# Kernel optimization log

Hardware: AMD Instinct MI355X
Metric: run time of the kernel (lower is better)

## Reference

```python
import jax, jax.numpy as jnp
from jax import lax
import numpy as np

IMG_H = IMG_W = 1024
STRIDE = 16
FH = FW = 64
C = 512
NA = 9
IOU_T = 0.7
NEG = -1e30
NUM_CLASSES = 21
FV = 4096
POOL = 7


def _make_anchor_map():
    scales = np.array([128.0, 256.0, 512.0])
    ratios = np.array([0.5, 1.0, 2.0])
    ah = (scales[:, None] * np.sqrt(ratios)[None, :]).reshape(-1)  # (9,)
    aw = (scales[:, None] / np.sqrt(ratios)[None, :]).reshape(-1)
    cy = (np.arange(FH) + 0.5) * STRIDE
    cx = (np.arange(FW) + 0.5) * STRIDE
    amap = np.zeros((FH, FW, NA, 4), np.float32)
    amap[..., 0] = cy[:, None, None]
    amap[..., 1] = cx[None, :, None]
    amap[..., 2] = ah
    amap[..., 3] = aw
    return amap.reshape(FH, FW, NA * 4)


def setup_inputs() -> dict:
    key = jax.random.key(0)
    ks = jax.random.split(key, 10)
    flat = POOL * POOL * C
    return {
        "feature_map": jax.random.normal(ks[0], (1, C, FH, FW), jnp.float32),
        "anchor_map": jnp.asarray(_make_anchor_map()),
        "anchor_valid_map": jnp.ones((FH, FW, NA), jnp.float32),
        "rpn_conv1_w": 0.01 * jax.random.normal(ks[1], (C, C, 3, 3), jnp.float32),
        "rpn_conv1_b": jnp.zeros((C,), jnp.float32),
        "rpn_cls_w": 0.01 * jax.random.normal(ks[2], (NA, C, 1, 1), jnp.float32),
        "rpn_cls_b": jnp.zeros((NA,), jnp.float32),
        "rpn_box_w": 0.01 * jax.random.normal(ks[3], (NA * 4, C, 1, 1), jnp.float32),
        "rpn_box_b": jnp.zeros((NA * 4,), jnp.float32),
        "fc1_w": 0.01 * jax.random.normal(ks[4], (FV, flat), jnp.float32),
        "fc1_b": jnp.zeros((FV,), jnp.float32),
        "fc2_w": 0.01 * jax.random.normal(ks[5], (FV, FV), jnp.float32),
        "fc2_b": jnp.zeros((FV,), jnp.float32),
        "cls_w": 0.01 * jax.random.normal(ks[6], (NUM_CLASSES, FV), jnp.float32),
        "cls_b": jnp.zeros((NUM_CLASSES,), jnp.float32),
        "reg_w": 0.001 * jax.random.normal(ks[7], (4 * (NUM_CLASSES - 1), FV), jnp.float32),
        "reg_b": jnp.zeros((4 * (NUM_CLASSES - 1),), jnp.float32),
        "max_proposals_pre_nms": 6000,
        "max_proposals_post_nms": 300,
    }


def _conv(x, w, b):
    y = lax.conv_general_dilated(x, w, (1, 1), 'SAME',
                                 dimension_numbers=('NCHW', 'OIHW', 'NCHW'))
    return y + b[None, :, None, None]


def _roi_pool(fm, rois):
    # fm: (C,H,W); rois: (N,4) as (x1,y1,x2,y2) in pixel coords (torchvision RoIPool semantics)
    Hh, Ww = fm.shape[1], fm.shape[2]
    s = 1.0 / STRIDE
    p = jnp.arange(POOL, dtype=fm.dtype)
    hi = jnp.arange(Hh, dtype=fm.dtype)
    wi = jnp.arange(Ww, dtype=fm.dtype)

    def one(roi):
        x1 = jnp.round(roi[0] * s); y1 = jnp.round(roi[1] * s)
        x2 = jnp.round(roi[2] * s); y2 = jnp.round(roi[3] * s)
        rw = jnp.maximum(x2 - x1 + 1.0, 1.0)
        rh = jnp.maximum(y2 - y1 + 1.0, 1.0)
        bh = rh / POOL; bw = rw / POOL
        hstart = jnp.clip(jnp.floor(p * bh) + y1, 0, Hh)
        hend = jnp.clip(jnp.ceil((p + 1) * bh) + y1, 0, Hh)
        wstart = jnp.clip(jnp.floor(p * bw) + x1, 0, Ww)
        wend = jnp.clip(jnp.ceil((p + 1) * bw) + x1, 0, Ww)
        mh = (hi[None, :] >= hstart[:, None]) & (hi[None, :] < hend[:, None])  # (7,H)
        mw = (wi[None, :] >= wstart[:, None]) & (wi[None, :] < wend[:, None])  # (7,W)
        # max over w per (c,h,pw), then max over h per (c,ph,pw)
        t1 = jnp.max(jnp.where(mw[None, None, :, :], fm[:, :, None, :], NEG), axis=-1)  # (C,H,7)
        t2 = jnp.max(jnp.where(mh[None, :, :, None], t1[:, None, :, :], NEG), axis=2)   # (C,7,7)
        return jnp.where(t2 < NEG / 2, 0.0, t2)  # empty bins -> 0

    return lax.map(one, rois)  # (N,C,7,7)


def reference(feature_map, anchor_map, anchor_valid_map,
              rpn_conv1_w, rpn_conv1_b, rpn_cls_w, rpn_cls_b, rpn_box_w, rpn_box_b,
              fc1_w, fc1_b, fc2_w, fc2_b, cls_w, cls_b, reg_w, reg_b,
              max_proposals_pre_nms, max_proposals_post_nms):
    # ---- RPN heads ----
    y = jax.nn.relu(_conv(feature_map, rpn_conv1_w, rpn_conv1_b))
    scores_map = jax.nn.sigmoid(_conv(y, rpn_cls_w, rpn_cls_b)).transpose(0, 2, 3, 1)   # (1,H,W,9)
    deltas_map = _conv(y, rpn_box_w, rpn_box_b).transpose(0, 2, 3, 1)                   # (1,H,W,36)

    # ---- proposals from anchors + deltas (allow_edge_proposals=True: keep all) ----
    anchors = anchor_map.reshape(-1, 4)        # (cy,cx,h,w)
    scores = scores_map.reshape(-1)
    deltas = deltas_map.reshape(-1, 4)         # (ty,tx,th,tw)
    ctr = anchors[:, 0:2] + deltas[:, 0:2] * anchors[:, 2:4]
    sz = anchors[:, 2:4] * jnp.exp(deltas[:, 2:4])
    boxes = jnp.concatenate([ctr - 0.5 * sz, ctr + 0.5 * sz], axis=1)  # (y1,x1,y2,x2)
    hi_clip = jnp.array([IMG_H - 1, IMG_W - 1, IMG_H - 1, IMG_W - 1], boxes.dtype)
    boxes = jnp.clip(boxes, 0.0, hi_clip)

    # ---- top-k pre-NMS ----
    sc_pre, idx = lax.top_k(scores, max_proposals_pre_nms)
    bx = boxes[idx]

    # ---- NMS (IoU 0.7), score-sorted sequential suppression ----
    area = (bx[:, 2] - bx[:, 0]) * (bx[:, 3] - bx[:, 1])
    yy1 = jnp.maximum(bx[:, None, 0], bx[None, :, 0])
    xx1 = jnp.maximum(bx[:, None, 1], bx[None, :, 1])
    yy2 = jnp.minimum(bx[:, None, 2], bx[None, :, 2])
    xx2 = jnp.minimum(bx[:, None, 3], bx[None, :, 3])
    inter = jnp.clip(yy2 - yy1, 0.0) * jnp.clip(xx2 - xx1, 0.0)
    iou = inter / (area[:, None] + area[None, :] - inter + 1e-8)
    n = max_proposals_pre_nms
    jidx = jnp.arange(n)

    def body(i, sup):
        return sup | ((~sup[i]) & (iou[i] > IOU_T) & (jidx > i))

    sup = lax.fori_loop(0, n, body, jnp.zeros((n,), bool))
    kept_scores = jnp.where(sup, -jnp.inf, sc_pre)
    _, idx2 = lax.top_k(kept_scores, max_proposals_post_nms)
    proposals = lax.stop_gradient(bx[idx2])  # (N,4) (y1,x1,y2,x2); detached as in original

    # ---- detector head: RoIPool + FC stack ----
    rois = proposals[:, jnp.array([1, 0, 3, 2])]       # -> (x1,y1,x2,y2)
    pooled = _roi_pool(feature_map[0], rois)           # (N,C,7,7)
    flat = pooled.reshape(pooled.shape[0], -1)
    h1 = jax.nn.relu(flat @ fc1_w.T + fc1_b)
    h2 = jax.nn.relu(h1 @ fc2_w.T + fc2_b)
    classes = jax.nn.softmax(h2 @ cls_w.T + cls_b, axis=1)          # (N,21)
    box_deltas = h2 @ reg_w.T + reg_b                               # (N,80)
    return (scores_map, deltas_map, proposals, classes, box_deltas)
```

## Files before the change

kernel.cpp:

```cpp
#include <hip/hip_runtime.h>
#include <stdint.h>

typedef float f32x4 __attribute__((ext_vector_type(4)));
typedef short s16x8 __attribute__((ext_vector_type(8)));
typedef unsigned long long u64;

__device__ __forceinline__ unsigned short f2bf(float f) {
  union { float f; unsigned u; } v; v.f = f;
  unsigned u = v.u;
  return (unsigned short)((u + 0x7FFFu + ((u >> 16) & 1u)) >> 16);
}
__device__ __forceinline__ float bf2f(unsigned short b) {
  union { unsigned u; float f; } v; v.u = ((unsigned)b) << 16; return v.f;
}

#define CONV_ICC 8
__global__ __launch_bounds__(256, 2) void k_conv3(const float* __restrict__ fm,
                                                  const float* __restrict__ w,
                                                  float* __restrict__ ypart) {
  __shared__ float Xs[CONV_ICC * 342];
  __shared__ float Ws[CONV_ICC * 9 * 64];
  int bid = blockIdx.x;
  int s = bid & 3, ocg = (bid >> 2) & 7, sp = bid >> 5;
  int h0 = (sp >> 2) * 16, w0 = (sp & 3) * 16;
  int oc0 = ocg * 64;
  int t = threadIdx.x;
  int g = t >> 5, p = t & 31;
  int row = p >> 1, colb = (p & 1) * 8;
  float acc[8][8] = {};
  int cbase = s * 128;
  for (int chunk = 0; chunk < 16; chunk++) {
    int c0 = cbase + chunk * CONV_ICC;
    for (int idx = t; idx < CONV_ICC * 324; idx += 256) {
      int ic = idx / 324, rem = idx - ic * 324;
      int r = rem / 18, cc = rem - r * 18;
      int gy = h0 + r - 1, gx = w0 + cc - 1;
      float v = 0.f;
      if ((unsigned)gy < 64u && (unsigned)gx < 64u) v = fm[(c0 + ic) * 4096 + gy * 64 + gx];
      Xs[ic * 342 + r * 19 + cc] = v;
    }
    for (int idx = t; idx < CONV_ICC * 9 * 64; idx += 256) {
      int oc = idx & 63, rest = idx >> 6;
      int ic = rest / 9, k = rest - ic * 9;
      Ws[idx] = w[(u64)(oc0 + oc) * 4608 + (c0 + ic) * 9 + k];
    }
    __syncthreads();
    for (int ic = 0; ic < CONV_ICC; ic++) {
      const float* xb = &Xs[ic * 342 + colb];
      float xr[3][10];
      #pragma unroll
      for (int r = 0; r < 3; r++)
        #pragma unroll
        for (int j = 0; j < 10; j++)
          xr[r][j] = xb[(row + r) * 19 + j];
      #pragma unroll
      for (int kh = 0; kh < 3; kh++) {
        #pragma unroll
        for (int kw = 0; kw < 3; kw++) {
          const float* wp = &Ws[(ic * 9 + kh * 3 + kw) * 64 + g * 8];
          f32x4 wa = *(const f32x4*)wp;
          f32x4 wb = *(const f32x4*)(wp + 4);
          float wv[8] = {wa.x, wa.y, wa.z, wa.w, wb.x, wb.y, wb.z, wb.w};
          #pragma unroll
          for (int o = 0; o < 8; o++) {
            #pragma unroll
            for (int j = 0; j < 8; j++) {
              acc[o][j] += wv[o] * xr[kh][kw + j];
            }
          }
        }
      }
    }
    __syncthreads();
  }
  float* yp = ypart + (u64)s * 2097152;
  #pragma unroll
  for (int j = 0; j < 8; j++) {
    int pxg = (h0 + row) * 64 + (w0 + colb + j);
    f32x4 v0, v1;
    v0.x = acc[0][j]; v0.y = acc[1][j]; v0.z = acc[2][j]; v0.w = acc[3][j];
    v1.x = acc[4][j]; v1.y = acc[5][j]; v1.z = acc[6][j]; v1.w = acc[7][j];
    f32x4* dst = (f32x4*)&yp[(u64)pxg * 512 + oc0 + g * 8];
    dst[0] = v0; dst[1] = v1;
  }
}

__global__ __launch_bounds__(256) void k_rpn1x1(const float* __restrict__ ypart,
                                                const float* __restrict__ conv_b,
                                                const float* __restrict__ cw, const float* __restrict__ cb,
                                                const float* __restrict__ bw, const float* __restrict__ bb,
                                                float* __restrict__ out_s, float* __restrict__ out_d) {
  __shared__ float Ys[16 * 516];
  int px0 = blockIdx.x * 16;
  int t = threadIdx.x;
  for (int c = t; c < 16 * 128; c += 256) {
    int p = c >> 7, seg = c & 127;
    u64 off = (u64)(px0 + p) * 512 + seg * 4;
    f32x4 v0 = *(const f32x4*)&ypart[off];
    f32x4 v1 = *(const f32x4*)&ypart[2097152 + off];
    f32x4 v2 = *(const f32x4*)&ypart[2 * 2097152 + off];
    f32x4 v3 = *(const f32x4*)&ypart[3 * (u64)2097152 + off];
    f32x4 b = *(const f32x4*)&conv_b[seg * 4];
    f32x4 r;
    r.x = fmaxf(v0.x + v1.x + v2.x + v3.x + b.x, 0.f);
    r.y = fmaxf(v0.y + v1.y + v2.y + v3.y + b.y, 0.f);
    r.z = fmaxf(v0.z + v1.z + v2.z + v3.z + b.z, 0.f);
    r.w = fmaxf(v0.w + v1.w + v2.w + v3.w + b.w, 0.f);
    *(f32x4*)&Ys[p * 516 + seg * 4] = r;
  }
  __syncthreads();
  int px = t & 15, og = t >> 4;
  const float* yr = &Ys[px * 516];
  for (int n = og; n < 45; n += 16) {
    const float* wr = (n < 9) ? &cw[n * 512] : &bw[(n - 9) * 512];
    float acc = 0.f;
    for (int k = 0; k < 512; k += 4) {
      f32x4 wv = *(const f32x4*)&wr[k];
      acc += wv.x * yr[k] + wv.y * yr[k + 1] + wv.z * yr[k + 2] + wv.w * yr[k + 3];
    }
    int gpx = px0 + px;
    if (n < 9) {
      float s = acc + cb[n];
      out_s[gpx * 9 + n] = 1.f / (1.f + expf(-s));
    } else {
      out_d[gpx * 36 + (n - 9)] = acc + bb[n - 9];
    }
  }
}

__global__ void k_decode(const float* __restrict__ sc, const float* __restrict__ dl,
                         const float* __restrict__ amap,
                         float* __restrict__ boxes, u64* __restrict__ keys) {
  int i = blockIdx.x * 256 + threadIdx.x;
  if (i >= 65536) return;
  if (i < 36864) {
    int px = i / 9, a = i - px * 9;
    const float* A = &amap[i * 4];
    const float* D = &dl[px * 36 + a * 4];
    float cy = A[0] + D[0] * A[2];
    float cx = A[1] + D[1] * A[3];
    float hh = A[2] * expf(D[2]);
    float ww = A[3] * expf(D[3]);
    float y1 = fminf(fmaxf(cy - 0.5f * hh, 0.f), 1023.f);
    float x1 = fminf(fmaxf(cx - 0.5f * ww, 0.f), 1023.f);
    float y2 = fminf(fmaxf(cy + 0.5f * hh, 0.f), 1023.f);
    float x2 = fminf(fmaxf(cx + 0.5f * ww, 0.f), 1023.f);
    f32x4 v; v.x = y1; v.y = x1; v.z = y2; v.w = x2;
    *(f32x4*)&boxes[i * 4] = v;
    unsigned bits = __float_as_uint(sc[i]);
    u64 key = ((u64)bits << 16) | (u64)(0xFFFFu - (unsigned)i);
    keys[i] = ~key;
  } else {
    keys[i] = ~0ull;
  }
}

__global__ __launch_bounds__(1024) void k_sort_local(u64* __restrict__ keys) {
  __shared__ u64 S[8192];
  int base = blockIdx.x * 8192;
  for (int i = threadIdx.x; i < 8192; i += 1024) S[i] = keys[base + i];
  __syncthreads();
  for (int k = 2; k <= 8192; k <<= 1) {
    for (int j = k >> 1; j > 0; j >>= 1) {
      for (int p = threadIdx.x; p < 4096; p += 1024) {
        int i = ((p & ~(j - 1)) << 1) | (p & (j - 1));
        int ix = i | j;
        bool up = (((base + i) & k) == 0);
        u64 a = S[i], c = S[ix];
        if ((a > c) == up) { S[i] = c; S[ix] = a; }
      }
      __syncthreads();
    }
  }
  for (int i = threadIdx.x; i < 8192; i += 1024) keys[base + i] = S[i];
}

__global__ void k_sort_global(u64* __restrict__ keys, int k, int j) {
  int p = blockIdx.x * 256 + threadIdx.x;
  int i = ((p & ~(j - 1)) << 1) | (p & (j - 1));
  int ix = i | j;
  bool up = ((i & k) == 0);
  u64 a = keys[i], c = keys[ix];
  if ((a > c) == up) { keys[i] = c; keys[ix] = a; }
}

__global__ __launch_bounds__(1024) void k_sort_merge(u64* __restrict__ keys, int k) {
  __shared__ u64 S[8192];
  int base = blockIdx.x * 8192;
  for (int i = threadIdx.x; i < 8192; i += 1024) S[i] = keys[base + i];
  __syncthreads();
  for (int j = 4096; j > 0; j >>= 1) {
    for (int p = threadIdx.x; p < 4096; p += 1024) {
      int i = ((p & ~(j - 1)) << 1) | (p & (j - 1));
      int ix = i | j;
      bool up = (((base + i) & k) == 0);
      u64 a = S[i], c = S[ix];
      if ((a > c) == up) { S[i] = c; S[ix] = a; }
    }
    __syncthreads();
  }
  for (int i = threadIdx.x; i < 8192; i += 1024) keys[base + i] = S[i];
}

__global__ void k_gather_sorted(const u64* __restrict__ keys, const float* __restrict__ boxes,
                                float* __restrict__ bx) {
  int p = blockIdx.x * 256 + threadIdx.x;
  if (p >= 6000) return;
  u64 key = ~keys[p];
  int idx = 0xFFFF - (int)(key & 0xFFFFull);
  *(f32x4*)&bx[p * 4] = *(const f32x4*)&boxes[idx * 4];
}

__global__ __launch_bounds__(128) void k_nms_mask(const float* __restrict__ bx, u64* __restrict__ mask) {
  int i = blockIdx.x;
  int w = threadIdx.x;
  if (w >= 94) return;
  f32x4 bi = *(const f32x4*)&bx[i * 4];
  float ai = (bi.z - bi.x) * (bi.w - bi.y);
  u64 m = 0;
  int j0 = w * 64;
  for (int b = 0; b < 64; b++) {
    int j = j0 + b;
    if (j >= 6000) break;
    if (j <= i) continue;
    f32x4 bj = *(const f32x4*)&bx[j * 4];
    float yy1 = fmaxf(bi.x, bj.x), xx1 = fmaxf(bi.y, bj.y);
    float yy2 = fminf(bi.z, bj.z), xx2 = fminf(bi.w, bj.w);
    float inter = fmaxf(yy2 - yy1, 0.f) * fmaxf(xx2 - xx1, 0.f);
    float aj = (bj.z - bj.x) * (bj.w - bj.y);
    float iou = inter / (ai + aj - inter + 1e-8f);
    if (iou > 0.7f) m |= (1ull << b);
  }
  mask[i * 94 + w] = m;
}

__global__ __launch_bounds__(64) void k_nms_scan(const u64* __restrict__ mask, int* __restrict__ sel) {
  int lane = threadIdx.x;
  u64 rem0 = 0, rem1 = 0;
  int nkeep = 0;
  u64 cur0[16], cur1[16], nxt0[16], nxt1[16];
  bool l30 = (lane < 30);
  #pragma unroll
  for (int r = 0; r < 16; r++) {
    cur0[r] = mask[r * 94 + lane];
    cur1[r] = l30 ? mask[r * 94 + 64 + lane] : 0ull;
  }
  for (int c0 = 0; c0 < 6000; c0 += 16) {
    int n0 = c0 + 16;
    if (n0 < 6000) {
      #pragma unroll
      for (int r = 0; r < 16; r++) {
        nxt0[r] = mask[(n0 + r) * 94 + lane];
        nxt1[r] = l30 ? mask[(n0 + r) * 94 + 64 + lane] : 0ull;
      }
    }
    #pragma unroll
    for (int r = 0; r < 16; r++) {
      int i = c0 + r;
      int wi = i >> 6, bi = i & 63;
      u64 wv = (wi < 64) ? __shfl(rem0, wi, 64) : __shfl(rem1, wi - 64, 64);
      if (!((wv >> bi) & 1ull)) {
        if (lane == 0 && nkeep < 300) sel[nkeep] = i;
        nkeep++;
        rem0 |= cur0[r]; rem1 |= cur1[r];
      }
    }
    if (nkeep >= 300) return;
    #pragma unroll
    for (int r = 0; r < 16; r++) { cur0[r] = nxt0[r]; cur1[r] = nxt1[r]; }
  }
  __shared__ u64 remS[94];
  remS[lane] = rem0;
  if (l30) remS[64 + lane] = rem1;
  __syncthreads();
  if (lane == 0) {
    int k = nkeep;
    for (int i = 0; i < 6000 && k < 300; i++) {
      if ((remS[i >> 6] >> (i & 63)) & 1ull) sel[k++] = i;
    }
  }
}

__global__ void k_gather_prop(const int* __restrict__ sel, const float* __restrict__ bx,
                              float* __restrict__ out_p, float* __restrict__ rois) {
  int r = blockIdx.x * 64 + threadIdx.x;
  if (r >= 300) return;
  int p = sel[r];
  float y1 = bx[p * 4 + 0], x1 = bx[p * 4 + 1], y2 = bx[p * 4 + 2], x2 = bx[p * 4 + 3];
  out_p[r * 4 + 0] = y1; out_p[r * 4 + 1] = x1; out_p[r * 4 + 2] = y2; out_p[r * 4 + 3] = x2;
  rois[r * 4 + 0] = x1; rois[r * 4 + 1] = y1; rois[r * 4 + 2] = x2; rois[r * 4 + 3] = y2;
}

__global__ __launch_bounds__(256) void k_roipool(const float* __restrict__ fm,
                                                 const float* __restrict__ rois,
                                                 unsigned short* __restrict__ pooled) {
  int roi = blockIdx.x / 98;
  int seg = blockIdx.x - roi * 98;
  __shared__ int hs[7], he[7], wls[7], wle[7];
  if (threadIdx.x < 28) {
    int kind = threadIdx.x / 7, p = threadIdx.x - kind * 7;
    float x1 = rintf(rois[roi * 4 + 0] * 0.0625f);
    float y1 = rintf(rois[roi * 4 + 1] * 0.0625f);
    float x2 = rintf(rois[roi * 4 + 2] * 0.0625f);
    float y2 = rintf(rois[roi * 4 + 3] * 0.0625f);
    float rw = fmaxf(x2 - x1 + 1.f, 1.f), rh = fmaxf(y2 - y1 + 1.f, 1.f);
    float bh = rh / 7.f, bw = rw / 7.f;
    float fp = (float)p;
    if (kind == 0) hs[p]  = (int)fminf(fmaxf(floorf(fp * bh) + y1, 0.f), 64.f);
    if (kind == 1) he[p]  = (int)fminf(fmaxf(ceilf((fp + 1.f) * bh) + y1, 0.f), 64.f);
    if (kind == 2) wls[p] = (int)fminf(fmaxf(floorf(fp * bw) + x1, 0.f), 64.f);
    if (kind == 3) wle[p] = (int)fminf(fmaxf(ceilf((fp + 1.f) * bw) + x1, 0.f), 64.f);
  }
  __syncthreads();
  int o = seg * 256 + threadIdx.x;
  int c = o / 49; int cell = o - c * 49;
  int ph = cell / 7, pw = cell - ph * 7;
  int y0 = hs[ph], y1e = he[ph], x0 = wls[pw], x1e = wle[pw];
  bool any = (y1e > y0) && (x1e > x0);
  float m = -1e30f;
  const float* base = &fm[c * 4096];
  for (int yy = y0; yy < y1e; yy++)
    for (int xx = x0; xx < x1e; xx++)
      m = fmaxf(m, base[yy * 64 + xx]);
  pooled[(u64)roi * 25088 + o] = f2bf(any ? m : 0.f);
}

__global__ __launch_bounds__(512) void k_gemm(const unsigned short* __restrict__ A,
                                              const float* __restrict__ B,
                                              float* __restrict__ Cpre,
                                              int K, int Kslice, int N) {
  __shared__ unsigned short As[320 * 40];
  int n0 = blockIdx.x * 128;
  int s = blockIdx.y;
  int t = threadIdx.x;
  int wave = t >> 6, lane = t & 63;
  int mg = wave & 1, ng = wave >> 1;
  int m0 = mg * 160;
  int n0w = n0 + ng * 32;
  int lr = lane & 15, lk = lane >> 4;
  f32x4 acc[10][2];
  #pragma unroll
  for (int mt = 0; mt < 10; mt++)
    for (int nt = 0; nt < 2; nt++) { acc[mt][nt].x = 0; acc[mt][nt].y = 0; acc[mt][nt].z = 0; acc[mt][nt].w = 0; }
  int kbeg = s * Kslice, kend = kbeg + Kslice;
  for (int k0 = kbeg; k0 < kend; k0 += 32) {
    for (int c = t; c < 1280; c += 512) {
      int m = c >> 2, seg = (c & 3) * 8;
      *(uint4*)&As[m * 40 + seg] = *(const uint4*)&A[(u64)m * K + k0 + seg];
    }
    __syncthreads();
    s16x8 bfrag[2];
    #pragma unroll
    for (int nt = 0; nt < 2; nt++) {
      const float* bp = &B[(u64)(n0w + nt * 16 + lr) * K + k0 + lk * 8];
      f32x4 b0 = *(const f32x4*)bp;
      f32x4 b1 = *(const f32x4*)(bp + 4);
      s16x8 f;
      f[0] = (short)f2bf(b0.x); f[1] = (short)f2bf(b0.y); f[2] = (short)f2bf(b0.z); f[3] = (short)f2bf(b0.w);
      f[4] = (short)f2bf(b1.x); f[5] = (short)f2bf(b1.y); f[6] = (short)f2bf(b1.z); f[7] = (short)f2bf(b1.w);
      bfrag[nt] = f;
    }
    #pragma unroll
    for (int mt = 0; mt < 10; mt++) {
      s16x8 afrag = *(const s16x8*)&As[(m0 + mt * 16 + lr) * 40 + lk * 8];
      acc[mt][0] = __builtin_amdgcn_mfma_f32_16x16x32_bf16(afrag, bfrag[0], acc[mt][0], 0, 0, 0);
      acc[mt][1] = __builtin_amdgcn_mfma_f32_16x16x32_bf16(afrag, bfrag[1], acc[mt][1], 0, 0, 0);
    }
    __syncthreads();
  }
  #pragma unroll
  for (int mt = 0; mt < 10; mt++)
    for (int nt = 0; nt < 2; nt++)
      for (int r = 0; r < 4; r++) {
        int m = m0 + mt * 16 + lk * 4 + r;
        int n = n0w + nt * 16 + lr;
        atomicAdd(&Cpre[(u64)m * N + n], acc[mt][nt][r]);
      }
}

__global__ void k_bias_relu_bf(const float* __restrict__ pre, const float* __restrict__ bias,
                               unsigned short* __restrict__ outb) {
  int i = blockIdx.x * 256 + threadIdx.x;
  float v = pre[i] + bias[i & 4095];
  outb[i] = f2bf(fmaxf(v, 0.f));
}

__global__ __launch_bounds__(128) void k_head(const unsigned short* __restrict__ h2,
                                              const float* __restrict__ cw, const float* __restrict__ cb,
                                              const float* __restrict__ rw, const float* __restrict__ rb,
                                              float* __restrict__ out_cls, float* __restrict__ out_reg) {
  __shared__ float Hs[4096];
  __shared__ float logits[101];
  __shared__ float es[21];
  int r = blockIdx.x, t = threadIdx.x;
  for (int c = t; c < 512; c += 128) {
    uint4 raw = *(const uint4*)&h2[(u64)r * 4096 + c * 8];
    unsigned short* sp = (unsigned short*)&raw;
    #pragma unroll
    for (int q = 0; q < 8; q++) Hs[c * 8 + q] = bf2f(sp[q]);
  }
  __syncthreads();
  for (int n = t; n < 101; n += 128) {
    const float* wrow = (n < 21) ? &cw[n * 4096] : &rw[(n - 21) * 4096];
    float acc = 0.f;
    for (int k = 0; k < 4096; k += 4) {
      f32x4 wv = *(const f32x4*)&wrow[k];
      acc += wv.x * Hs[k] + wv.y * Hs[k + 1] + wv.z * Hs[k + 2] + wv.w * Hs[k + 3];
    }
    acc += (n < 21) ? cb[n] : rb[n - 21];
    logits[n] = acc;
  }
  __syncthreads();
  if (t < 21) {
    float mx = logits[0];
    for (int q = 1; q < 21; q++) mx = fmaxf(mx, logits[q]);
    es[t] = expf(logits[t] - mx);
  }
  __syncthreads();
  if (t < 21) {
    float sum = 0.f;
    for (int q = 0; q < 21; q++) sum += es[q];
    out_cls[r * 21 + t] = es[t] / sum;
  }
  if (t >= 21 && t < 101) out_reg[r * 80 + (t - 21)] = logits[t];
}

extern "C" void kernel_launch(void* const* d_in, const int* in_sizes, int n_in,
                              void* d_out, int out_size, void* d_ws, size_t ws_size,
                              hipStream_t stream) {
  (void)in_sizes; (void)n_in; (void)out_size; (void)ws_size;
  const float* fm     = (const float*)d_in[0];
  const float* amap   = (const float*)d_in[1];
  const float* conv_w = (const float*)d_in[3];
  const float* conv_b = (const float*)d_in[4];
  const float* cls_w  = (const float*)d_in[5];
  const float* cls_b  = (const float*)d_in[6];
  const float* box_w  = (const float*)d_in[7];
  const float* box_b  = (const float*)d_in[8];
  const float* fc1_w  = (const float*)d_in[9];
  const float* fc1_b  = (const float*)d_in[10];
  const float* fc2_w  = (const float*)d_in[11];
  const float* fc2_b  = (const float*)d_in[12];
  const float* cw     = (const float*)d_in[13];
  const float* cbias  = (const float*)d_in[14];
  const float* rw     = (const float*)d_in[15];
  const float* rbias  = (const float*)d_in[16];

  float* out_s = (float*)d_out;
  float* out_d = out_s + 36864;
  float* out_p = out_d + 147456;
  float* out_c = out_p + 1200;
  float* out_r = out_c + 6300;

  char* ws = (char*)d_ws;
  float* ypart = (float*)(ws + 0);
  u64*   mask  = (u64*)  (ws + 0);
  unsigned short* pooled = (unsigned short*)(ws + 4718592);
  float* boxes = (float*)(ws + 20971520);
  u64*   keys  = (u64*)  (ws + 21561344);
  float* bx    = (float*)(ws + 22085632);
  int*   sel   = (int*)  (ws + 22181632);
  float* rois  = (float*)(ws + 22182912);
  float* h1pre = (float*)(ws + 22282240);
  unsigned short* h1bf = (unsigned short*)(ws + 27525120);
  float* h2pre = h1pre;
  unsigned short* h2bf = (unsigned short*)(ws + 30146560);

  k_conv3<<<512, 256, 0, stream>>>(fm, conv_w, ypart);
  k_rpn1x1<<<256, 256, 0, stream>>>(ypart, conv_b, cls_w, cls_b, box_w, box_b, out_s, out_d);
  k_decode<<<256, 256, 0, stream>>>(out_s, out_d, amap, boxes, keys);

  k_sort_local<<<8, 1024, 0, stream>>>(keys);
  for (int k = 16384; k <= 65536; k <<= 1) {
    for (int j = k >> 1; j >= 8192; j >>= 1)
      k_sort_global<<<128, 256, 0, stream>>>(keys, k, j);
    k_sort_merge<<<8, 1024, 0, stream>>>(keys, k);
  }

  k_gather_sorted<<<24, 256, 0, stream>>>(keys, boxes, bx);
  k_nms_mask<<<6000, 128, 0, stream>>>(bx, mask);
  k_nms_scan<<<1, 64, 0, stream>>>(mask, sel);
  k_gather_prop<<<5, 64, 0, stream>>>(sel, bx, out_p, rois);

  hipMemsetAsync((char*)pooled + (size_t)300 * 25088 * 2, 0, (size_t)20 * 25088 * 2, stream);
  hipMemsetAsync(h1pre, 0, (size_t)320 * 4096 * 4, stream);

  k_roipool<<<300 * 98, 256, 0, stream>>>(fm, rois, pooled);

  k_gemm<<<dim3(32, 8), 512, 0, stream>>>(pooled, fc1_w, h1pre, 25088, 3136, 4096);
  k_bias_relu_bf<<<5120, 256, 0, stream>>>(h1pre, fc1_b, h1bf);
  hipMemsetAsync(h2pre, 0, (size_t)320 * 4096 * 4, stream);
  k_gemm<<<dim3(32, 8), 512, 0, stream>>>(h1bf, fc2_w, h2pre, 4096, 512, 4096);
  k_bias_relu_bf<<<5120, 256, 0, stream>>>(h2pre, fc2_b, h2bf);
  k_head<<<300, 128, 0, stream>>>(h2bf, cw, cbias, rw, rbias, out_c, out_r);
}
```

Baseline: 1.077 ms.

## Load GEMM A fragments directly from global memory, dropping LDS staging and barriers

The FC GEMM kernel no longer stages the activation tile in shared memory. Each wave loads its A fragments straight from global memory into registers and issues all loads before the MFMAs, with no __syncthreads. The block index is flattened so that consecutive blocks take different K-slices of the same N tile, which may improve L2 locality for A. The cost is redundant global/L2 reads of A across the four N-waves and higher register pressure.

After: 1.260 ms. 17.0% more time.

```diff
diff --git a/kernel.cpp b/kernel.cpp
--- a/kernel.cpp
+++ b/kernel.cpp
@@ -325,13 +325,13 @@
   pooled[(u64)roi * 25088 + o] = f2bf(any ? m : 0.f);
 }
 
-__global__ __launch_bounds__(512) void k_gemm(const unsigned short* __restrict__ A,
-                                              const float* __restrict__ B,
-                                              float* __restrict__ Cpre,
-                                              int K, int Kslice, int N) {
-  __shared__ unsigned short As[320 * 40];
-  int n0 = blockIdx.x * 128;
-  int s = blockIdx.y;
+__global__ __launch_bounds__(512) void k_gemm2(const unsigned short* __restrict__ A,
+                                               const float* __restrict__ B,
+                                               float* __restrict__ Cpre,
+                                               int K, int Kslice, int N) {
+  int bid = blockIdx.x;
+  int s = bid & 7, nb = bid >> 3;
+  int n0 = nb * 128;
   int t = threadIdx.x;
   int wave = t >> 6, lane = t & 63;
   int mg = wave & 1, ng = wave >> 1;
@@ -342,31 +342,37 @@
   #pragma unroll
   for (int mt = 0; mt < 10; mt++)
     for (int nt = 0; nt < 2; nt++) { acc[mt][nt].x = 0; acc[mt][nt].y = 0; acc[mt][nt].z = 0; acc[mt][nt].w = 0; }
+  const unsigned short* Ab = A + (u64)(m0 + lr) * K + lk * 8;
+  const float* Bb = B + (u64)(n0w + lr) * K + lk * 8;
+  u64 rowA = (u64)16 * K;
   int kbeg = s * Kslice, kend = kbeg + Kslice;
   for (int k0 = kbeg; k0 < kend; k0 += 32) {
-    for (int c = t; c < 1280; c += 512) {
-      int m = c >> 2, seg = (c & 3) * 8;
-      *(uint4*)&As[m * 40 + seg] = *(const uint4*)&A[(u64)m * K + k0 + seg];
-    }
-    __syncthreads();
+    s16x8 af[10];
+    #pragma unroll
+    for (int mt = 0; mt < 10; mt++)
+      af[mt] = *(const s16x8*)&Ab[(u64)mt * rowA + k0];
+    f32x4 b0[2], b1[2];
+    #pragma unroll
+    for (int nt = 0; nt < 2; nt++) {
+      const float* bp = &Bb[(u64)nt * rowA + k0];
+      b0[nt] = *(const f32x4*)bp;
+      b1[nt] = *(const f32x4*)(bp + 4);
+    }
     s16x8 bfrag[2];
     #pragma unroll
     for (int nt = 0; nt < 2; nt++) {
-      const float* bp = &B[(u64)(n0w + nt * 16 + lr) * K + k0 + lk * 8];
-      f32x4 b0 = *(const f32x4*)bp;
-      f32x4 b1 = *(const f32x4*)(bp + 4);
       s16x8 f;
-      f[0] = (short)f2bf(b0.x); f[1] = (short)f2bf(b0.y); f[2] = (short)f2bf(b0.z); f[3] = (short)f2bf(b0.w);
-      f[4] = (short)f2bf(b1.x); f[5] = (short)f2bf(b1.y); f[6] = (short)f2bf(b1.z); f[7] = (short)f2bf(b1.w);
+      f[0] = (short)f2bf(b0[nt].x); f[1] = (short)f2bf(b0[nt].y);
+      f[2] = (short)f2bf(b0[nt].z); f[3] = (short)f2bf(b0[nt].w);
+      f[4] = (short)f2bf(b1[nt].x); f[5] = (short)f2bf(b1[nt].y);
+      f[6] = (short)f2bf(b1[nt].z); f[7] = (short)f2bf(b1[nt].w);
       bfrag[nt] = f;
     }
     #pragma unroll
     for (int mt = 0; mt < 10; mt++) {
-      s16x8 afrag = *(const s16x8*)&As[(m0 + mt * 16 + lr) * 40 + lk * 8];
-      acc[mt][0] = __builtin_amdgcn_mfma_f32_16x16x32_bf16(afrag, bfrag[0], acc[mt][0], 0, 0, 0);
-      acc[mt][1] = __builtin_amdgcn_mfma_f32_16x16x32_bf16(afrag, bfrag[1], acc[mt][1], 0, 0, 0);
-    }
-    __syncthreads();
+      acc[mt][0] = __builtin_amdgcn_mfma_f32_16x16x32_bf16(af[mt], bfrag[0], acc[mt][0], 0, 0, 0);
+      acc[mt][1] = __builtin_amdgcn_mfma_f32_16x16x32_bf16(af[mt], bfrag[1], acc[mt][1], 0, 0, 0);
+    }
   }
   #pragma unroll
   for (int mt = 0; mt < 10; mt++)
@@ -487,10 +493,10 @@
 
   k_roipool<<<300 * 98, 256, 0, stream>>>(fm, rois, pooled);
 
-  k_gemm<<<dim3(32, 8), 512, 0, stream>>>(pooled, fc1_w, h1pre, 25088, 3136, 4096);
+  k_gemm2<<<256, 512, 0, stream>>>(pooled, fc1_w, h1pre, 25088, 3136, 4096);
   k_bias_relu_bf<<<5120, 256, 0, stream>>>(h1pre, fc1_b, h1bf);
   hipMemsetAsync(h2pre, 0, (size_t)320 * 4096 * 4, stream);
-  k_gemm<<<dim3(32, 8), 512, 0, stream>>>(h1bf, fc2_w, h2pre, 4096, 512, 4096);
+  k_gemm2<<<256, 512, 0, stream>>>(h1bf, fc2_w, h2pre, 4096, 512, 4096);
   k_bias_relu_bf<<<5120, 256, 0, stream>>>(h2pre, fc2_b, h2bf);
   k_head<<<300, 128, 0, stream>>>(h2bf, cw, cbias, rw, rbias, out_c, out_r);
 }
```

## Double-buffer FC GEMM with register prefetch and shared-memory B staging

Applied to the files above, without the earlier changes.

Replaces the FC GEMM with a version that uses a K-step of 64 and double-buffered shared memory for both A and B. Global loads for the next tile are issued into registers before the MFMA work on the current tile, then written to the alternate buffer, so one barrier per step replaces two. B is now converted to bf16 once per element and staged in LDS, so waves no longer each convert their own fragments from global memory. The cost is more LDS per block and more registers, with a 2-blocks-per-SM launch bound that may cause spills. The new code requires Kslice to be a multiple of 64, which holds for both calls (3136 and 512).

After: 1.004 ms. -6.8%, faster.

```diff
diff --git a/kernel.cpp b/kernel.cpp
--- a/kernel.cpp
+++ b/kernel.cpp
@@ -325,55 +325,112 @@
   pooled[(u64)roi * 25088 + o] = f2bf(any ? m : 0.f);
 }
 
-__global__ __launch_bounds__(512) void k_gemm(const unsigned short* __restrict__ A,
-                                              const float* __restrict__ B,
-                                              float* __restrict__ Cpre,
-                                              int K, int Kslice, int N) {
-  __shared__ unsigned short As[320 * 40];
+__global__ __launch_bounds__(512, 2) void k_gemm3(const unsigned short* __restrict__ A,
+                                                  const float* __restrict__ B,
+                                                  float* __restrict__ Cpre,
+                                                  int K, int Kslice, int N) {
+  __shared__ uint4 Ab[2][2560];
+  __shared__ uint4 Bb[2][1024];
   int n0 = blockIdx.x * 128;
   int s = blockIdx.y;
   int t = threadIdx.x;
   int wave = t >> 6, lane = t & 63;
   int mg = wave & 1, ng = wave >> 1;
   int m0 = mg * 160;
-  int n0w = n0 + ng * 32;
   int lr = lane & 15, lk = lane >> 4;
+
+  int am[5], aks[5];
+  #pragma unroll
+  for (int i = 0; i < 5; i++) { int idx = t + i * 512; am[i] = idx % 320; aks[i] = idx / 320; }
+  int brow = t >> 2, bpart = t & 3;
+  const float* gB = &B[(u64)(n0 + brow) * K + bpart * 16];
+
   f32x4 acc[10][2];
   #pragma unroll
   for (int mt = 0; mt < 10; mt++)
     for (int nt = 0; nt < 2; nt++) { acc[mt][nt].x = 0; acc[mt][nt].y = 0; acc[mt][nt].z = 0; acc[mt][nt].w = 0; }
-  int kbeg = s * Kslice, kend = kbeg + Kslice;
-  for (int k0 = kbeg; k0 < kend; k0 += 32) {
-    for (int c = t; c < 1280; c += 512) {
-      int m = c >> 2, seg = (c & 3) * 8;
-      *(uint4*)&As[m * 40 + seg] = *(const uint4*)&A[(u64)m * K + k0 + seg];
+
+  int kbeg = s * Kslice;
+  int nt_iters = Kslice >> 6;
+  uint4 Araw[5];
+  f32x4 Braw[4];
+
+  #pragma unroll
+  for (int i = 0; i < 5; i++)
+    Araw[i] = *(const uint4*)&A[(u64)am[i] * K + kbeg + aks[i] * 8];
+  #pragma unroll
+  for (int q = 0; q < 4; q++)
+    Braw[q] = *(const f32x4*)&gB[kbeg + q * 4];
+  #pragma unroll
+  for (int i = 0; i < 5; i++) Ab[0][t + i * 512] = Araw[i];
+  {
+    float fv[16] = {Braw[0].x, Braw[0].y, Braw[0].z, Braw[0].w,
+                    Braw[1].x, Braw[1].y, Braw[1].z, Braw[1].w,
+                    Braw[2].x, Braw[2].y, Braw[2].z, Braw[2].w,
+                    Braw[3].x, Braw[3].y, Braw[3].z, Braw[3].w};
+    #pragma unroll
+    for (int h = 0; h < 2; h++) {
+      s16x8 pk;
+      #pragma unroll
+      for (int j = 0; j < 8; j++) pk[j] = (short)f2bf(fv[h * 8 + j]);
+      *(s16x8*)&Bb[0][(bpart * 2 + h) * 128 + brow] = pk;
+    }
+  }
+  __syncthreads();
+
+  int cur = 0;
+  int k0 = kbeg;
+  for (int it = 0; it < nt_iters; it++) {
+    bool pf = (it + 1 < nt_iters);
+    if (pf) {
+      int kn = k0 + 64;
+      #pragma unroll
+      for (int i = 0; i < 5; i++)
+        Araw[i] = *(const uint4*)&A[(u64)am[i] * K + kn + aks[i] * 8];
+      #pragma unroll
+      for (int q = 0; q < 4; q++)
+        Braw[q] = *(const f32x4*)&gB[kn + q * 4];
+    }
+    const unsigned short* ab = (const unsigned short*)Ab[cur];
+    const unsigned short* bb = (const unsigned short*)Bb[cur];
+    #pragma unroll
+    for (int ksub = 0; ksub < 2; ksub++) {
+      int ks = ksub * 4 + lk;
+      s16x8 bf0 = *(const s16x8*)&bb[(u64)(ks * 128 + ng * 32 + lr) * 8];
+      s16x8 bf1 = *(const s16x8*)&bb[(u64)(ks * 128 + ng * 32 + 16 + lr) * 8];
+      #pragma unroll
+      for (int mt = 0; mt < 10; mt++) {
+        s16x8 af = *(const s16x8*)&ab[(u64)(ks * 320 + m0 + mt * 16 + lr) * 8];
+        acc[mt][0] = __builtin_amdgcn_mfma_f32_16x16x32_bf16(af, bf0, acc[mt][0], 0, 0, 0);
+        acc[mt][1] = __builtin_amdgcn_mfma_f32_16x16x32_bf16(af, bf1, acc[mt][1], 0, 0, 0);
+      }
+    }
+    if (pf) {
+      #pragma unroll
+      for (int i = 0; i < 5; i++) Ab[cur ^ 1][t + i * 512] = Araw[i];
+      float fv[16] = {Braw[0].x, Braw[0].y, Braw[0].z, Braw[0].w,
+                      Braw[1].x, Braw[1].y, Braw[1].z, Braw[1].w,
+                      Braw[2].x, Braw[2].y, Braw[2].z, Braw[2].w,
+                      Braw[3].x, Braw[3].y, Braw[3].z, Braw[3].w};
+      #pragma unroll
+      for (int h = 0; h < 2; h++) {
+        s16x8 pk;
+        #pragma unroll
+        for (int j = 0; j < 8; j++) pk[j] = (short)f2bf(fv[h * 8 + j]);
+        *(s16x8*)&Bb[cur ^ 1][(bpart * 2 + h) * 128 + brow] = pk;
+      }
     }
     __syncthreads();
-    s16x8 bfrag[2];
-    #pragma unroll
-    for (int nt = 0; nt < 2; nt++) {
-      const float* bp = &B[(u64)(n0w + nt * 16 + lr) * K + k0 + lk * 8];
-      f32x4 b0 = *(const f32x4*)bp;
-      f32x4 b1 = *(const f32x4*)(bp + 4);
-      s16x8 f;
-      f[0] = (short)f2bf(b0.x); f[1] = (short)f2bf(b0.y); f[2] = (short)f2bf(b0.z); f[3] = (short)f2bf(b0.w);
-      f[4] = (short)f2bf(b1.x); f[5] = (short)f2bf(b1.y); f[6] = (short)f2bf(b1.z); f[7] = (short)f2bf(b1.w);
-      bfrag[nt] = f;
-    }
-    #pragma unroll
-    for (int mt = 0; mt < 10; mt++) {
-      s16x8 afrag = *(const s16x8*)&As[(m0 + mt * 16 + lr) * 40 + lk * 8];
-      acc[mt][0] = __builtin_amdgcn_mfma_f32_16x16x32_bf16(afrag, bfrag[0], acc[mt][0], 0, 0, 0);
-      acc[mt][1] = __builtin_amdgcn_mfma_f32_16x16x32_bf16(afrag, bfrag[1], acc[mt][1], 0, 0, 0);
-    }
-    __syncthreads();
-  }
+    cur ^= 1;
+    k0 += 64;
+  }
+
   #pragma unroll
   for (int mt = 0; mt < 10; mt++)
     for (int nt = 0; nt < 2; nt++)
       for (int r = 0; r < 4; r++) {
         int m = m0 + mt * 16 + lk * 4 + r;
-        int n = n0w + nt * 16 + lr;
+        int n = n0 + ng * 32 + nt * 16 + lr;
         atomicAdd(&Cpre[(u64)m * N + n], acc[mt][nt][r]);
       }
 }
@@ -487,10 +544,10 @@
 
   k_roipool<<<300 * 98, 256, 0, stream>>>(fm, rois, pooled);
 
-  k_gemm<<<dim3(32, 8), 512, 0, stream>>>(pooled, fc1_w, h1pre, 25088, 3136, 4096);
+  k_gemm3<<<dim3(32, 8), 512, 0, stream>>>(pooled, fc1_w, h1pre, 25088, 3136, 4096);
   k_bias_relu_bf<<<5120, 256, 0, stream>>>(h1pre, fc1_b, h1bf);
   hipMemsetAsync(h2pre, 0, (size_t)320 * 4096 * 4, stream);
-  k_gemm<<<dim3(32, 8), 512, 0, stream>>>(h1bf, fc2_w, h2pre, 4096, 512, 4096);
+  k_gemm3<<<dim3(32, 8), 512, 0, stream>>>(h1bf, fc2_w, h2pre, 4096, 512, 4096);
   k_bias_relu_bf<<<5120, 256, 0, stream>>>(h2pre, fc2_b, h2bf);
   k_head<<<300, 128, 0, stream>>>(h2bf, cw, cbias, rw, rbias, out_c, out_r);
 }
```
